# Performance work log

Measured on AMD Instinct MI355X. Metric: run time of the kernel, lower is better.

## Reference

```python
import jax, jax.numpy as jnp
import numpy as np

B, T, D, H = 64, 1024, 512, 512

def setup_inputs() -> dict:
    key = jax.random.key(0)
    k1, k2, k3, k4 = jax.random.split(key, 4)
    x = jax.random.normal(k1, (B, T, D), dtype=jnp.float32)
    # Keras LSTM weights: kernel [D, 4H], recurrent_kernel [H, 4H], bias [4H]
    # gate order: i, f, c(g), o
    kernel = jax.random.normal(k2, (D, 4 * H), dtype=jnp.float32) * 0.05
    recurrent_kernel = jax.random.normal(k3, (H, 4 * H), dtype=jnp.float32) * 0.05
    bias = jax.random.normal(k4, (4 * H,), dtype=jnp.float32) * 0.05
    return {"x": x, "kernel": kernel, "recurrent_kernel": recurrent_kernel, "bias": bias}

def reference(x, kernel, recurrent_kernel, bias):
    # Precompute input projections for all timesteps: [B, T, 4H]
    xW = jnp.einsum('btd,dg->btg', x, kernel) + bias
    xW_t = jnp.transpose(xW, (1, 0, 2))  # [T, B, 4H] for scan over time
    h0 = jnp.zeros((x.shape[0], recurrent_kernel.shape[0]), dtype=x.dtype)
    c0 = jnp.zeros_like(h0)

    def step(carry, xw):
        h, c = carry
        z = xw + h @ recurrent_kernel  # [B, 4H]
        i, f, g, o = jnp.split(z, 4, axis=-1)
        i = jax.nn.sigmoid(i)
        f = jax.nn.sigmoid(f)
        g = jnp.tanh(g)
        o = jax.nn.sigmoid(o)
        c_new = f * c + i * g
        h_new = o * jnp.tanh(c_new)
        return (h_new, c_new), None

    (h_final, _), _ = jax.lax.scan(step, (h0, c0), xW_t)
    return h_final  # [B, H]
```

## Files before the change

kernel.cpp:

```cpp
#include <hip/hip_runtime.h>


#define B_  64
#define T_  1024
#define D_  512
#define H_  512
#define G4H 2048

typedef _Float16 half8 __attribute__((ext_vector_type(8)));
typedef float    f32x4 __attribute__((ext_vector_type(4)));
typedef unsigned long long ull;

static __device__ __forceinline__ float sigm(float x) { return 1.f / (1.f + __expf(-x)); }
static __device__ __forceinline__ float tanh_(float x) {
    float xc = fminf(fmaxf(x, -15.f), 15.f);
    float e  = __expf(2.f * xc);
    return (e - 1.f) / (e + 1.f);
}
static __device__ __forceinline__ float lo16f(unsigned u) {
    return (float)__builtin_bit_cast(_Float16, (unsigned short)(u & 0xffffu));
}
static __device__ __forceinline__ float hi16f(unsigned u) {
    return (float)__builtin_bit_cast(_Float16, (unsigned short)(u >> 16));
}

__global__ void init_kernel(const float* __restrict__ Wk, _Float16* __restrict__ WkT) {
    int idx = blockIdx.x * blockDim.x + threadIdx.x;
    int total = D_ * G4H;
    int stride = gridDim.x * blockDim.x;
    for (int i = idx; i < total; i += stride) {
        int k = i >> 11;
        int n = i & (G4H - 1);
        WkT[(size_t)n * D_ + k] = (_Float16)Wk[i];
    }
}

__global__ __launch_bounds__(256) void gemm_xw(const float* __restrict__ x,
                                               const _Float16* __restrict__ WkT,
                                               const float* __restrict__ bias,
                                               _Float16* __restrict__ xw,
                                               int tbase) {
    __shared__ _Float16 As[64][40];
    __shared__ _Float16 Bst[64][40];
    const int tid  = threadIdx.x;
    const int lane = tid & 63;
    const int wave = tid >> 6;
    const int l15  = lane & 15;
    const int quad = lane >> 4;
    const int b     = blockIdx.z;
    const int n0    = blockIdx.x * 64;
    const int tloc0 = blockIdx.y * 64;

    const float* xbase = x + ((size_t)b * T_ + (tbase + tloc0)) * D_;
    f32x4 acc[4];
#pragma unroll
    for (int i = 0; i < 4; ++i) acc[i] = (f32x4){0.f, 0.f, 0.f, 0.f};

    const int ai = tid >> 2, ac = tid & 3;
    const int bn = tid >> 2, bq = tid & 3;

    for (int kb = 0; kb < 16; ++kb) {
        __syncthreads();
        const float* ap = xbase + (size_t)ai * D_ + kb * 32 + ac * 8;
        f32x4 av0 = *(const f32x4*)ap;
        f32x4 av1 = *(const f32x4*)(ap + 4);
        half8 ah = { (_Float16)av0.x, (_Float16)av0.y, (_Float16)av0.z, (_Float16)av0.w,
                     (_Float16)av1.x, (_Float16)av1.y, (_Float16)av1.z, (_Float16)av1.w };
        *(half8*)&As[ai][ac * 8] = ah;
        half8 bv = *(const half8*)(WkT + (size_t)(n0 + bn) * D_ + kb * 32 + bq * 8);
        *(half8*)&Bst[bn][bq * 8] = bv;
        __syncthreads();

        half8 afrag = *(const half8*)&As[16 * wave + l15][quad * 8];
#pragma unroll
        for (int nt = 0; nt < 4; ++nt) {
            half8 bfrag = *(const half8*)&Bst[nt * 16 + l15][quad * 8];
            acc[nt] = __builtin_amdgcn_mfma_f32_16x16x32_f16(afrag, bfrag, acc[nt], 0, 0, 0);
        }
    }
#pragma unroll
    for (int nt = 0; nt < 4; ++nt)
#pragma unroll
        for (int r = 0; r < 4; ++r) {
            int tt  = tloc0 + 16 * wave + quad * 4 + r;
            int col = n0 + nt * 16 + l15;
            xw[((size_t)tt * B_ + b) * G4H + col] = (_Float16)(acc[nt][r] + bias[col]);
        }
}

__global__ __launch_bounds__(512, 1) void lstm_scan(const _Float16* __restrict__ xw,
                                                    const float* __restrict__ Wr,
                                                    unsigned* __restrict__ hbuf,
                                                    float* __restrict__ cio,
                                                    float* __restrict__ out,
                                                    int t0, int t1) {
    const int w    = blockIdx.x;
    const int g    = w & 3;
    const int s    = w >> 2;
    const int u0   = s * 64;
    const int tid  = threadIdx.x;
    const int lane = tid & 63;
    const int wave = tid >> 6;
    const int l15  = lane & 15;
    const int quad = lane >> 4;
    const int gv   = wave >> 1;
    const int hv   = wave & 1;

    half8 bfrag[2][16];
#pragma unroll
    for (int ct = 0; ct < 2; ++ct) {
        const int col = gv * H_ + u0 + hv * 32 + ct * 16 + l15;
#pragma unroll
        for (int kt = 0; kt < 16; ++kt) {
            half8 v;
#pragma unroll
            for (int j = 0; j < 8; ++j)
                v[j] = (_Float16)Wr[(size_t)(kt * 32 + quad * 8 + j) * G4H + col];
            bfrag[ct][kt] = v;
        }
    }

    const int rho  = tid >> 5;
    const int jj   = tid & 31;
    const int brow = g * 16 + rho;
    const int un0  = u0 + 2 * jj;
    float c0 = 0.f, c1 = 0.f;
    if (t0 != 0) {
        c0 = cio[(size_t)brow * H_ + un0];
        c1 = cio[(size_t)brow * H_ + un0 + 1];
    }

    __shared__ _Float16 hS[16][520];
    __shared__ float    zS[16][260];

    const size_t slotSz = (size_t)B_ * H_;

    for (int t = t0; t < t1; ++t) {
        const unsigned* xwd = (const unsigned*)(xw + ((size_t)(t - t0) * B_ + brow) * G4H);
        const int dbase = s * 32 + jj;
        unsigned xwi = xwd[0 * 256 + dbase];
        unsigned xwf = xwd[1 * 256 + dbase];
        unsigned xwg = xwd[2 * 256 + dbase];
        unsigned xwo = xwd[3 * 256 + dbase];

        if (t > 0) {
            const ull* src = (const ull*)(hbuf + (size_t)((t - 1) % 3) * slotSz)
                             + (size_t)(g * 16) * 256 + tid;
            const unsigned tgt = (unsigned)(t & 0xffff);
            const ull expect = ((ull)tgt << 16) | ((ull)tgt << 48);
            ull v[8];
            int guard = 0;
            while (true) {
                ull diff = 0;
#pragma unroll
                for (int k = 0; k < 8; ++k)
                    v[k] = __hip_atomic_load(src + (size_t)k * 512,
                                             __ATOMIC_RELAXED, __HIP_MEMORY_SCOPE_AGENT);
#pragma unroll
                for (int k = 0; k < 8; ++k)
                    diff |= (v[k] ^ expect) & 0xffff0000ffff0000ull;
                if (diff == 0) break;
                if (++guard > (1 << 14)) break;
                __builtin_amdgcn_s_sleep(1);
            }
#pragma unroll
            for (int k = 0; k < 8; ++k) {
                int idx = k * 512 + tid;
                int row = idx >> 8, col = idx & 255;
                unsigned p = (unsigned)(v[k] & 0xffffu) | (((unsigned)(v[k] >> 32)) << 16);
                *(unsigned*)&hS[row][2 * col] = p;
            }
        }
        __syncthreads();

        f32x4 a0 = {0.f,0.f,0.f,0.f}, a1 = a0, b0 = a0, b1 = a0;
        if (t > 0) {
#pragma unroll
            for (int kt = 0; kt < 16; kt += 2) {
                half8 af0 = *(const half8*)&hS[l15][kt * 32 + quad * 8];
                half8 af1 = *(const half8*)&hS[l15][(kt + 1) * 32 + quad * 8];
                a0 = __builtin_amdgcn_mfma_f32_16x16x32_f16(af0, bfrag[0][kt],     a0, 0, 0, 0);
                a1 = __builtin_amdgcn_mfma_f32_16x16x32_f16(af0, bfrag[1][kt],     a1, 0, 0, 0);
                b0 = __builtin_amdgcn_mfma_f32_16x16x32_f16(af1, bfrag[0][kt + 1], b0, 0, 0, 0);
                b1 = __builtin_amdgcn_mfma_f32_16x16x32_f16(af1, bfrag[1][kt + 1], b1, 0, 0, 0);
            }
        }
        f32x4 z0 = a0 + b0, z1 = a1 + b1;
        {
            const int bc = gv * 64 + hv * 32;
#pragma unroll
            for (int r = 0; r < 4; ++r) {
                zS[quad * 4 + r][bc + l15]      = z0[r];
                zS[quad * 4 + r][bc + 16 + l15] = z1[r];
            }
        }
        __syncthreads();

        float zi0 = zS[rho][2*jj]       + lo16f(xwi), zi1 = zS[rho][2*jj + 1]       + hi16f(xwi);
        float zf0 = zS[rho][64 + 2*jj]  + lo16f(xwf), zf1 = zS[rho][64 + 2*jj + 1]  + hi16f(xwf);
        float zg0 = zS[rho][128 + 2*jj] + lo16f(xwg), zg1 = zS[rho][128 + 2*jj + 1] + hi16f(xwg);
        float zo0 = zS[rho][192 + 2*jj] + lo16f(xwo), zo1 = zS[rho][192 + 2*jj + 1] + hi16f(xwo);

        c0 = sigm(zf0) * c0 + sigm(zi0) * tanh_(zg0);
        c1 = sigm(zf1) * c1 + sigm(zi1) * tanh_(zg1);
        float h0 = sigm(zo0) * tanh_(c0);
        float h1 = sigm(zo1) * tanh_(c1);

        const unsigned tagw = ((unsigned)((t + 1) & 0xffff)) << 16;
        unsigned d0 = (unsigned)__builtin_bit_cast(unsigned short, (_Float16)h0) | tagw;
        unsigned d1 = (unsigned)__builtin_bit_cast(unsigned short, (_Float16)h1) | tagw;
        ull wv = (ull)d0 | ((ull)d1 << 32);
        __hip_atomic_store((ull*)(hbuf + (size_t)(t % 3) * slotSz) + (size_t)brow * 256 + (un0 >> 1),
                           wv, __ATOMIC_RELAXED, __HIP_MEMORY_SCOPE_AGENT);

        if (t == T_ - 1) {
            out[(size_t)brow * H_ + un0]     = h0;
            out[(size_t)brow * H_ + un0 + 1] = h1;
        }
    }
    cio[(size_t)brow * H_ + un0]     = c0;
    cio[(size_t)brow * H_ + un0 + 1] = c1;
}

extern "C" void kernel_launch(void* const* d_in, const int* in_sizes, int n_in,
                              void* d_out, int out_size, void* d_ws, size_t ws_size,
                              hipStream_t stream) {
    const float* x    = (const float*)d_in[0];
    const float* Wk   = (const float*)d_in[1];
    const float* Wr   = (const float*)d_in[2];
    const float* bias = (const float*)d_in[3];
    float* out = (float*)d_out;

    char* ws = (char*)d_ws;
    _Float16* WkT   = (_Float16*)(ws + 1024);
    unsigned* hbuf  = (unsigned*)(ws + 1024 + 2097152);
    float*    cio   = (float*)  (ws + 1024 + 2097152 + 393216);
    const size_t fixed = 1024 + 2097152 + 393216 + 131072;
    _Float16* xw    = (_Float16*)(ws + fixed);

    size_t avail = (ws_size > fixed) ? ws_size - fixed : 0;
    int ct = 0;
    const int cands[5] = {1024, 512, 256, 128, 64};
    for (int i = 0; i < 5; ++i) {
        if ((size_t)cands[i] * (size_t)(B_ * G4H * 2) <= avail) { ct = cands[i]; break; }
    }
    if (ct == 0) {
        hipMemsetAsync(d_out, 0, (size_t)out_size * 4, stream);
        return;
    }

    init_kernel<<<512, 256, 0, stream>>>(Wk, WkT);
    for (int t0 = 0; t0 < T_; t0 += ct) {
        gemm_xw<<<dim3(32, ct / 64, B_), 256, 0, stream>>>(x, WkT, bias, xw, t0);
        lstm_scan<<<32, 512, 0, stream>>>(xw, Wr, hbuf, cio, out, t0, t0 + ct);
    }
}
```

Baseline: 3.736 ms.

## Keep all four gates per wave in registers, halve scan blocks, drop zS exchange

The recurrent scan now runs on 16 blocks, and each wave computes all four gates for 16 hidden units, holding four gate B-fragments in registers. The gate nonlinearities can then be applied straight from the MFMA accumulators, which removes the shared-memory z exchange and one __syncthreads per timestep. The xW buffer is relaid out as [t][gate-col][batch] so each lane loads a half4 of batch values, and the GEMM tiles over batch per timestep. The spin-wait now keeps two overlapping batches of polling loads in flight with no sleep. The cost is twice the register use for the weight fragments and fewer blocks spread across the CUs.

```diff
diff --git a/kernel.cpp b/kernel.cpp
--- a/kernel.cpp
+++ b/kernel.cpp
@@ -8,6 +8,7 @@
 #define G4H 2048
 
 typedef _Float16 half8 __attribute__((ext_vector_type(8)));
+typedef _Float16 half4 __attribute__((ext_vector_type(4)));
 typedef float    f32x4 __attribute__((ext_vector_type(4)));
 typedef unsigned long long ull;
 
@@ -16,12 +17,6 @@
     float xc = fminf(fmaxf(x, -15.f), 15.f);
     float e  = __expf(2.f * xc);
     return (e - 1.f) / (e + 1.f);
-}
-static __device__ __forceinline__ float lo16f(unsigned u) {
-    return (float)__builtin_bit_cast(_Float16, (unsigned short)(u & 0xffffu));
-}
-static __device__ __forceinline__ float hi16f(unsigned u) {
-    return (float)__builtin_bit_cast(_Float16, (unsigned short)(u >> 16));
 }
 
 __global__ void init_kernel(const float* __restrict__ Wk, _Float16* __restrict__ WkT) {
@@ -47,11 +42,9 @@
     const int wave = tid >> 6;
     const int l15  = lane & 15;
     const int quad = lane >> 4;
-    const int b     = blockIdx.z;
-    const int n0    = blockIdx.x * 64;
-    const int tloc0 = blockIdx.y * 64;
-
-    const float* xbase = x + ((size_t)b * T_ + (tbase + tloc0)) * D_;
+    const int n0   = blockIdx.x * 64;
+    const int t    = tbase + blockIdx.y;
+
     f32x4 acc[4];
 #pragma unroll
     for (int i = 0; i < 4; ++i) acc[i] = (f32x4){0.f, 0.f, 0.f, 0.f};
@@ -61,7 +54,7 @@
 
     for (int kb = 0; kb < 16; ++kb) {
         __syncthreads();
-        const float* ap = xbase + (size_t)ai * D_ + kb * 32 + ac * 8;
+        const float* ap = x + ((size_t)ai * T_ + t) * D_ + kb * 32 + ac * 8;
         f32x4 av0 = *(const f32x4*)ap;
         f32x4 av1 = *(const f32x4*)(ap + 4);
         half8 ah = { (_Float16)av0.x, (_Float16)av0.y, (_Float16)av0.z, (_Float16)av0.w,
@@ -78,14 +71,15 @@
             acc[nt] = __builtin_amdgcn_mfma_f32_16x16x32_f16(afrag, bfrag, acc[nt], 0, 0, 0);
         }
     }
-#pragma unroll
-    for (int nt = 0; nt < 4; ++nt)
-#pragma unroll
-        for (int r = 0; r < 4; ++r) {
-            int tt  = tloc0 + 16 * wave + quad * 4 + r;
-            int col = n0 + nt * 16 + l15;
-            xw[((size_t)tt * B_ + b) * G4H + col] = (_Float16)(acc[nt][r] + bias[col]);
-        }
+    const int trow = (int)blockIdx.y;
+#pragma unroll
+    for (int nt = 0; nt < 4; ++nt) {
+        int col = n0 + nt * 16 + l15;
+        float bs = bias[col];
+        half4 hv = { (_Float16)(acc[nt][0] + bs), (_Float16)(acc[nt][1] + bs),
+                     (_Float16)(acc[nt][2] + bs), (_Float16)(acc[nt][3] + bs) };
+        *(half4*)(xw + ((size_t)trow * G4H + col) * B_ + 16 * wave + quad * 4) = hv;
+    }
 }
 
 __global__ __launch_bounds__(512, 1) void lstm_scan(const _Float16* __restrict__ xw,
@@ -97,129 +91,145 @@
     const int w    = blockIdx.x;
     const int g    = w & 3;
     const int s    = w >> 2;
-    const int u0   = s * 64;
     const int tid  = threadIdx.x;
     const int lane = tid & 63;
     const int wave = tid >> 6;
     const int l15  = lane & 15;
     const int quad = lane >> 4;
-    const int gv   = wave >> 1;
-    const int hv   = wave & 1;
-
-    half8 bfrag[2][16];
-#pragma unroll
-    for (int ct = 0; ct < 2; ++ct) {
-        const int col = gv * H_ + u0 + hv * 32 + ct * 16 + l15;
+    const int ut   = s * 128 + wave * 16;
+    const int unit = ut + l15;
+
+    half8 bfrag[4][16];
+#pragma unroll
+    for (int gate = 0; gate < 4; ++gate) {
+        const int col = gate * H_ + unit;
 #pragma unroll
         for (int kt = 0; kt < 16; ++kt) {
             half8 v;
 #pragma unroll
             for (int j = 0; j < 8; ++j)
                 v[j] = (_Float16)Wr[(size_t)(kt * 32 + quad * 8 + j) * G4H + col];
-            bfrag[ct][kt] = v;
-        }
-    }
-
-    const int rho  = tid >> 5;
-    const int jj   = tid & 31;
-    const int brow = g * 16 + rho;
-    const int un0  = u0 + 2 * jj;
-    float c0 = 0.f, c1 = 0.f;
+            bfrag[gate][kt] = v;
+        }
+    }
+
+    float c[4] = {0.f, 0.f, 0.f, 0.f};
     if (t0 != 0) {
-        c0 = cio[(size_t)brow * H_ + un0];
-        c1 = cio[(size_t)brow * H_ + un0 + 1];
+#pragma unroll
+        for (int r = 0; r < 4; ++r)
+            c[r] = cio[(size_t)(g * 16 + quad * 4 + r) * H_ + unit];
     }
 
     __shared__ _Float16 hS[16][520];
-    __shared__ float    zS[16][260];
 
     const size_t slotSz = (size_t)B_ * H_;
+    const ull MASK = 0xffff0000ffff0000ull;
 
     for (int t = t0; t < t1; ++t) {
-        const unsigned* xwd = (const unsigned*)(xw + ((size_t)(t - t0) * B_ + brow) * G4H);
-        const int dbase = s * 32 + jj;
-        unsigned xwi = xwd[0 * 256 + dbase];
-        unsigned xwf = xwd[1 * 256 + dbase];
-        unsigned xwg = xwd[2 * 256 + dbase];
-        unsigned xwo = xwd[3 * 256 + dbase];
+        const _Float16* xb = xw + (size_t)(t - t0) * G4H * B_;
+        const int b0 = g * 16 + quad * 4;
+        half4 xg[4];
+#pragma unroll
+        for (int gate = 0; gate < 4; ++gate)
+            xg[gate] = *(const half4*)(xb + ((size_t)(gate * H_ + unit)) * B_ + b0);
 
         if (t > 0) {
             const ull* src = (const ull*)(hbuf + (size_t)((t - 1) % 3) * slotSz)
-                             + (size_t)(g * 16) * 256 + tid;
+                             + (size_t)g * 4096 + tid;
             const unsigned tgt = (unsigned)(t & 0xffff);
             const ull expect = ((ull)tgt << 16) | ((ull)tgt << 48);
-            ull v[8];
+            ull v0[8], v1[8];
+#pragma unroll
+            for (int k = 0; k < 8; ++k)
+                v0[k] = __hip_atomic_load(src + (size_t)k * 512, __ATOMIC_RELAXED, __HIP_MEMORY_SCOPE_AGENT);
+#pragma unroll
+            for (int k = 0; k < 8; ++k)
+                v1[k] = __hip_atomic_load(src + (size_t)k * 512, __ATOMIC_RELAXED, __HIP_MEMORY_SCOPE_AGENT);
             int guard = 0;
             while (true) {
-                ull diff = 0;
+                ull d = 0;
+#pragma unroll
+                for (int k = 0; k < 8; ++k) d |= (v0[k] ^ expect) & MASK;
+                if (d == 0) break;
 #pragma unroll
                 for (int k = 0; k < 8; ++k)
-                    v[k] = __hip_atomic_load(src + (size_t)k * 512,
-                                             __ATOMIC_RELAXED, __HIP_MEMORY_SCOPE_AGENT);
+                    v0[k] = __hip_atomic_load(src + (size_t)k * 512, __ATOMIC_RELAXED, __HIP_MEMORY_SCOPE_AGENT);
+                d = 0;
+#pragma unroll
+                for (int k = 0; k < 8; ++k) d |= (v1[k] ^ expect) & MASK;
+                if (d == 0) {
+#pragma unroll
+                    for (int k = 0; k < 8; ++k) v0[k] = v1[k];
+                    break;
+                }
 #pragma unroll
                 for (int k = 0; k < 8; ++k)
-                    diff |= (v[k] ^ expect) & 0xffff0000ffff0000ull;
-                if (diff == 0) break;
+                    v1[k] = __hip_atomic_load(src + (size_t)k * 512, __ATOMIC_RELAXED, __HIP_MEMORY_SCOPE_AGENT);
                 if (++guard > (1 << 14)) break;
-                __builtin_amdgcn_s_sleep(1);
             }
 #pragma unroll
             for (int k = 0; k < 8; ++k) {
                 int idx = k * 512 + tid;
-                int row = idx >> 8, col = idx & 255;
-                unsigned p = (unsigned)(v[k] & 0xffffu) | (((unsigned)(v[k] >> 32)) << 16);
-                *(unsigned*)&hS[row][2 * col] = p;
+                int row = idx >> 8, cu = idx & 255;
+                unsigned p = (unsigned)(v0[k] & 0xffffu) | (((unsigned)(v0[k] >> 32)) << 16);
+                *(unsigned*)&hS[row][2 * cu] = p;
             }
         }
         __syncthreads();
 
-        f32x4 a0 = {0.f,0.f,0.f,0.f}, a1 = a0, b0 = a0, b1 = a0;
+        f32x4 acc[4];
+#pragma unroll
+        for (int i = 0; i < 4; ++i) acc[i] = (f32x4){0.f, 0.f, 0.f, 0.f};
         if (t > 0) {
 #pragma unroll
-            for (int kt = 0; kt < 16; kt += 2) {
-                half8 af0 = *(const half8*)&hS[l15][kt * 32 + quad * 8];
-                half8 af1 = *(const half8*)&hS[l15][(kt + 1) * 32 + quad * 8];
-                a0 = __builtin_amdgcn_mfma_f32_16x16x32_f16(af0, bfrag[0][kt],     a0, 0, 0, 0);
-                a1 = __builtin_amdgcn_mfma_f32_16x16x32_f16(af0, bfrag[1][kt],     a1, 0, 0, 0);
-                b0 = __builtin_amdgcn_mfma_f32_16x16x32_f16(af1, bfrag[0][kt + 1], b0, 0, 0, 0);
-                b1 = __builtin_amdgcn_mfma_f32_16x16x32_f16(af1, bfrag[1][kt + 1], b1, 0, 0, 0);
+            for (int kt = 0; kt < 16; ++kt) {
+                half8 af = *(const half8*)&hS[l15][kt * 32 + quad * 8];
+                acc[0] = __builtin_amdgcn_mfma_f32_16x16x32_f16(af, bfrag[0][kt], acc[0], 0, 0, 0);
+                acc[1] = __builtin_amdgcn_mfma_f32_16x16x32_f16(af, bfrag[1][kt], acc[1], 0, 0, 0);
+                acc[2] = __builtin_amdgcn_mfma_f32_16x16x32_f16(af, bfrag[2][kt], acc[2], 0, 0, 0);
+                acc[3] = __builtin_amdgcn_mfma_f32_16x16x32_f16(af, bfrag[3][kt], acc[3], 0, 0, 0);
             }
         }
-        f32x4 z0 = a0 + b0, z1 = a1 + b1;
-        {
-            const int bc = gv * 64 + hv * 32;
-#pragma unroll
-            for (int r = 0; r < 4; ++r) {
-                zS[quad * 4 + r][bc + l15]      = z0[r];
-                zS[quad * 4 + r][bc + 16 + l15] = z1[r];
-            }
-        }
-        __syncthreads();
-
-        float zi0 = zS[rho][2*jj]       + lo16f(xwi), zi1 = zS[rho][2*jj + 1]       + hi16f(xwi);
-        float zf0 = zS[rho][64 + 2*jj]  + lo16f(xwf), zf1 = zS[rho][64 + 2*jj + 1]  + hi16f(xwf);
-        float zg0 = zS[rho][128 + 2*jj] + lo16f(xwg), zg1 = zS[rho][128 + 2*jj + 1] + hi16f(xwg);
-        float zo0 = zS[rho][192 + 2*jj] + lo16f(xwo), zo1 = zS[rho][192 + 2*jj + 1] + hi16f(xwo);
-
-        c0 = sigm(zf0) * c0 + sigm(zi0) * tanh_(zg0);
-        c1 = sigm(zf1) * c1 + sigm(zi1) * tanh_(zg1);
-        float h0 = sigm(zo0) * tanh_(c0);
-        float h1 = sigm(zo1) * tanh_(c1);
 
         const unsigned tagw = ((unsigned)((t + 1) & 0xffff)) << 16;
-        unsigned d0 = (unsigned)__builtin_bit_cast(unsigned short, (_Float16)h0) | tagw;
-        unsigned d1 = (unsigned)__builtin_bit_cast(unsigned short, (_Float16)h1) | tagw;
-        ull wv = (ull)d0 | ((ull)d1 << 32);
-        __hip_atomic_store((ull*)(hbuf + (size_t)(t % 3) * slotSz) + (size_t)brow * 256 + (un0 >> 1),
-                           wv, __ATOMIC_RELAXED, __HIP_MEMORY_SCOPE_AGENT);
+        unsigned dtag[4];
+        float h[4];
+#pragma unroll
+        for (int r = 0; r < 4; ++r) {
+            float zi = acc[0][r] + (float)xg[0][r];
+            float zf = acc[1][r] + (float)xg[1][r];
+            float zg = acc[2][r] + (float)xg[2][r];
+            float zo = acc[3][r] + (float)xg[3][r];
+            c[r] = sigm(zf) * c[r] + sigm(zi) * tanh_(zg);
+            h[r] = sigm(zo) * tanh_(c[r]);
+            dtag[r] = (unsigned)__builtin_bit_cast(unsigned short, (_Float16)h[r]) | tagw;
+        }
+
+        unsigned ptag[4];
+#pragma unroll
+        for (int r = 0; r < 4; ++r) ptag[r] = __shfl_xor((int)dtag[r], 1);
+        ull* slotw = (ull*)(hbuf + (size_t)(t % 3) * slotSz);
+        const int pairb = (ut >> 1) + (l15 >> 1);
+        const int r0 = (lane & 1) ? 2 : 0;
+#pragma unroll
+        for (int i = 0; i < 2; ++i) {
+            int r = r0 + i;
+            unsigned lo = (lane & 1) ? ptag[r] : dtag[r];
+            unsigned hi = (lane & 1) ? dtag[r] : ptag[r];
+            ull wv = (ull)lo | ((ull)hi << 32);
+            __hip_atomic_store(slotw + (size_t)(g * 16 + quad * 4 + r) * 256 + pairb,
+                               wv, __ATOMIC_RELAXED, __HIP_MEMORY_SCOPE_AGENT);
+        }
 
         if (t == T_ - 1) {
-            out[(size_t)brow * H_ + un0]     = h0;
-            out[(size_t)brow * H_ + un0 + 1] = h1;
-        }
-    }
-    cio[(size_t)brow * H_ + un0]     = c0;
-    cio[(size_t)brow * H_ + un0 + 1] = c1;
+#pragma unroll
+            for (int r = 0; r < 4; ++r)
+                out[(size_t)(g * 16 + quad * 4 + r) * H_ + unit] = h[r];
+        }
+    }
+#pragma unroll
+    for (int r = 0; r < 4; ++r)
+        cio[(size_t)(g * 16 + quad * 4 + r) * H_ + unit] = c[r];
 }
 
 extern "C" void kernel_launch(void* const* d_in, const int* in_sizes, int n_in,
@@ -251,7 +261,7 @@
 
     init_kernel<<<512, 256, 0, stream>>>(Wk, WkT);
     for (int t0 = 0; t0 < T_; t0 += ct) {
-        gemm_xw<<<dim3(32, ct / 64, B_), 256, 0, stream>>>(x, WkT, bias, xw, t0);
-        lstm_scan<<<32, 512, 0, stream>>>(xw, Wr, hbuf, cio, out, t0, t0 + ct);
-    }
-}
+        gemm_xw<<<dim3(32, ct), 256, 0, stream>>>(x, WkT, bias, xw, t0);
+        lstm_scan<<<16, 512, 0, stream>>>(xw, Wr, hbuf, cio, out, t0, t0 + ct);
+    }
+}
```

New measurement: 12.34 ms. +230.3%, slower.
